# Optimization experiments

Measured on AMD Instinct MI355X. Metric: run time of the kernel, lower is better.

## Reference

```python
import jax, jax.numpy as jnp
import numpy as np
from jax import lax

REL_THR = 0.7
REP_THR = 0.7
EPS = 1e-12


def setup_inputs() -> dict:
    key = jax.random.key(0)
    k1, k2, k3 = jax.random.split(key, 3)
    C, H, W = 128, 768, 1024
    return {
        "features": jax.random.normal(k1, (1, C, H, W), dtype=jnp.float32),
        "clf_w": jax.random.normal(k2, (C, 2), dtype=jnp.float32) * 0.1,
        "clf_b": jnp.zeros((2,), dtype=jnp.float32),
        "sal_w": jax.random.normal(k3, (C, 2), dtype=jnp.float32) * 0.1,
        "sal_b": jnp.zeros((2,), dtype=jnp.float32),
        "max_keypoints": 5000,
    }


def _maxpool3(x):
    # 3x3 stride-1 same-padded max pool on [B, 1, H, W]
    return lax.reduce_window(
        x, -jnp.inf, lax.max,
        window_dimensions=(1, 1, 3, 3),
        window_strides=(1, 1, 1, 1),
        padding=((0, 0), (0, 0), (1, 1), (1, 1)),
    )


def reference(features, clf_w, clf_b, sal_w, sal_b, max_keypoints):
    B, C, H, W = features.shape  # B == 1
    f2 = features ** 2
    # 1x1-conv heads (clf -> reliability logits, sal -> repeatability logits)
    urel = jnp.einsum('bchw,co->bohw', f2, clf_w) + clf_b[None, :, None, None]
    urep = jnp.einsum('bchw,co->bohw', f2, sal_w) + sal_b[None, :, None, None]
    reliability = jax.nn.softmax(urel, axis=1)[:, 1:2]    # [1,1,H,W]
    repeatability = jax.nn.softmax(urep, axis=1)[:, 1:2]  # [1,1,H,W]

    # NonMaxSuppression: local-max + dual threshold
    maxima = (repeatability == _maxpool3(repeatability))
    maxima &= (repeatability >= REP_THR)
    maxima &= (reliability >= REL_THR)

    scores_map = (reliability * repeatability)[0, 0]      # [H, W]
    flat = jnp.where(maxima[0, 0], scores_map, -jnp.inf).reshape(-1)
    scores, idx = lax.top_k(flat, max_keypoints)          # fixed-shape top-K
    y = idx // W
    x = idx % W
    keypoints = jnp.stack([x, y], axis=-1).astype(jnp.float32)  # [K, 2]

    # L2-normalized descriptors gathered at keypoints
    norm = jnp.sqrt(jnp.sum(features * features, axis=1, keepdims=True))
    desc = features / jnp.maximum(norm, EPS)              # [1,C,H,W]
    descriptors = desc[0, :, y, x].T                      # [K, C]
    return keypoints, scores, descriptors
```

## Files before the change

kernel.cpp:

```cpp
#include <hip/hip_runtime.h>
#include <math.h>

#define HH   768
#define WW   1024
#define CC   128
#define HWN  (HH*WW)
#define KTOP 5000
#define CAND_CAP 204800
#define SEL_CAP  8192
#define NBINS    4096
#define BIN_BASE 0x3E800u

#define OFF_REP    0ull
#define OFF_SMAP   3145728ull
#define OFF_CAND   6291456ull
#define OFF_HIST   (OFF_CAND + (unsigned long long)CAND_CAP*8ull)
#define OFF_CTR    (OFF_HIST + (unsigned long long)NBINS*4ull)
#define OFF_SEL    (OFF_CTR + 64ull)
#define OFF_SORTED (OFF_SEL + (unsigned long long)SEL_CAP*8ull)

__device__ __forceinline__ float exp_cr(float x) {
    return (float)::exp((double)x);
}

__global__ void k_zero(unsigned* hist, unsigned* ctr, unsigned* sorted32) {
    int t = blockIdx.x * blockDim.x + threadIdx.x;
    if (t < NBINS) hist[t] = 0u;
    if (t < 16) ctr[t] = 0u;
    if (t < KTOP * 2) sorted32[t] = 0u;
}

__global__ __launch_bounds__(256, 4) void k_maps(const float* __restrict__ f,
                       const float* __restrict__ cw, const float* __restrict__ cb,
                       const float* __restrict__ sw, const float* __restrict__ sb,
                       float* __restrict__ rep, float* __restrict__ smap) {
    __shared__ float w0[CC], w1[CC], w2[CC], w3[CC];
    int t = threadIdx.x;
    if (t < CC) {
        w0[t] = cw[2*t];  w1[t] = cw[2*t+1];
        w2[t] = sw[2*t];  w3[t] = sw[2*t+1];
    }
    __syncthreads();
    int p0 = (blockIdx.x * blockDim.x + t) * 4;
    if (p0 >= HWN) return;
    const float4* fp = (const float4*)(f + p0);
    const long step = HWN / 4;

    float a0[4] = {0,0,0,0}, a1[4] = {0,0,0,0}, a2[4] = {0,0,0,0}, a3[4] = {0,0,0,0};
    float4 A[4], B[4];
    #pragma unroll
    for (int k = 0; k < 4; ++k) A[k] = fp[(long)k * step];

    #define FMA4(REG, CBASE)                                             \
        _Pragma("unroll")                                                \
        for (int k = 0; k < 4; ++k) {                                    \
            int c = (CBASE) + k;                                         \
            float W0 = w0[c], W1 = w1[c], W2 = w2[c], W3 = w3[c];        \
            float vv[4] = {REG[k].x, REG[k].y, REG[k].z, REG[k].w};      \
            _Pragma("unroll")                                            \
            for (int j = 0; j < 4; ++j) {                                \
                float f2 = vv[j] * vv[j];                                \
                a0[j] = fmaf(f2, W0, a0[j]);                             \
                a1[j] = fmaf(f2, W1, a1[j]);                             \
                a2[j] = fmaf(f2, W2, a2[j]);                             \
                a3[j] = fmaf(f2, W3, a3[j]);                             \
            }                                                            \
        }

    for (int c0 = 0; c0 < CC; c0 += 8) {
        #pragma unroll
        for (int k = 0; k < 4; ++k) B[k] = fp[(long)(c0 + 4 + k) * step];
        FMA4(A, c0)
        if (c0 + 8 < CC) {
            #pragma unroll
            for (int k = 0; k < 4; ++k) A[k] = fp[(long)(c0 + 8 + k) * step];
        }
        FMA4(B, c0 + 4)
    }
    #undef FMA4

    float cb0 = cb[0], cb1 = cb[1], sb0 = sb[0], sb1 = sb[1];
    float rp4[4], sm4[4];
    #pragma unroll
    for (int j = 0; j < 4; ++j) {
        float u0 = a0[j] + cb0, u1 = a1[j] + cb1;
        float v0 = a2[j] + sb0, v1 = a3[j] + sb1;
        float mr  = fmaxf(u0, u1);
        float er0 = exp_cr(u0 - mr);
        float er1 = exp_cr(u1 - mr);
        float rel = er1 / (er0 + er1);
        float mp  = fmaxf(v0, v1);
        float ep0 = exp_cr(v0 - mp);
        float ep1 = exp_cr(v1 - mp);
        float rp  = ep1 / (ep0 + ep1);
        rp4[j] = rp;
        sm4[j] = (rel >= 0.7f) ? rel * rp : -1.0f;
    }
    *(float4*)(rep + p0)  = make_float4(rp4[0], rp4[1], rp4[2], rp4[3]);
    *(float4*)(smap + p0) = make_float4(sm4[0], sm4[1], sm4[2], sm4[3]);
}

__global__ void k_nms(const float* __restrict__ rep, const float* __restrict__ smap,
                      unsigned long long* __restrict__ cand, unsigned* __restrict__ ctr,
                      unsigned* __restrict__ hist) {
    int p = blockIdx.x * blockDim.x + threadIdx.x;
    if (p >= HWN) return;
    float r = rep[p];
    if (!(r >= 0.7f)) return;
    float s = smap[p];
    if (!(s >= 0.f)) return;
    int x = p & (WW - 1), y = p >> 10;
    float m = -INFINITY;
    if (y > 0) {
        const float* rr = rep + p - WW;
        if (x > 0)      m = fmaxf(m, rr[-1]);
        m = fmaxf(m, rr[0]);
        if (x < WW - 1) m = fmaxf(m, rr[1]);
    }
    if (x > 0)      m = fmaxf(m, rep[p - 1]);
    if (x < WW - 1) m = fmaxf(m, rep[p + 1]);
    if (y < HH - 1) {
        const float* rr = rep + p + WW;
        if (x > 0)      m = fmaxf(m, rr[-1]);
        m = fmaxf(m, rr[0]);
        if (x < WW - 1) m = fmaxf(m, rr[1]);
    }
    if (r < m) return;
    unsigned pos = atomicAdd(&ctr[0], 1u);
    if (pos < CAND_CAP) {
        unsigned sb = __float_as_uint(s);
        cand[pos] = ((unsigned long long)sb << 32) |
                    (unsigned long long)(0xFFFFFFFFu - (unsigned)p);
        int bin = (int)(sb >> 12) - (int)BIN_BASE;
        bin = bin < 0 ? 0 : (bin > NBINS - 1 ? NBINS - 1 : bin);
        atomicAdd(&hist[bin], 1u);
    }
}

__global__ __launch_bounds__(1024) void k_thr(const unsigned* __restrict__ hist,
                                              unsigned* __restrict__ ctr) {
    __shared__ unsigned ps[1024];
    __shared__ int best;
    int t = threadIdx.x;
    if (t == 0) best = -1;
    unsigned h[4];
    unsigned s = 0;
    #pragma unroll
    for (int k = 0; k < 4; ++k) { h[k] = hist[t*4 + k]; s += h[k]; }
    ps[t] = s;
    __syncthreads();
    for (int off = 1; off < 1024; off <<= 1) {
        unsigned v = (t + off < 1024) ? ps[t + off] : 0u;
        __syncthreads();
        ps[t] += v;
        __syncthreads();
    }
    unsigned above4 = (t < 1023) ? ps[t + 1] : 0u;
    int local = -1;
    unsigned cum = above4;
    #pragma unroll
    for (int k = 3; k >= 0; --k) {
        cum += h[k];
        if (local < 0 && cum >= KTOP) local = t*4 + k;
    }
    if (local >= 0) atomicMax(&best, local);
    __syncthreads();
    if (t == 0) {
        int b = best;
        ctr[2] = (b <= 0) ? 0u : ((unsigned)(b + (int)BIN_BASE) << 12);
    }
}

__global__ void k_select(const unsigned long long* __restrict__ cand,
                         unsigned* __restrict__ ctr, unsigned long long* __restrict__ sel) {
    unsigned n = ctr[0]; if (n > CAND_CAP) n = CAND_CAP;
    unsigned thr = ctr[2];
    int stride = gridDim.x * blockDim.x;
    for (unsigned i = blockIdx.x * blockDim.x + threadIdx.x; i < n; i += stride) {
        unsigned long long k = cand[i];
        if ((unsigned)(k >> 32) >= thr) {
            unsigned pos = atomicAdd(&ctr[1], 1u);
            if (pos < SEL_CAP) sel[pos] = k;
        }
    }
}

__global__ __launch_bounds__(256) void k_rank(const unsigned long long* __restrict__ sel,
                                              const unsigned* __restrict__ ctr,
                                              unsigned long long* __restrict__ sorted) {
    unsigned n = ctr[1]; if (n > SEL_CAP) n = SEL_CAP;
    int wave = (blockIdx.x * 256 + threadIdx.x) >> 6;
    int lane = threadIdx.x & 63;
    int base = wave * 8;
    if (base >= (int)n) return;
    unsigned long long my[8];
    unsigned cnt[8] = {0,0,0,0,0,0,0,0};
    #pragma unroll
    for (int e = 0; e < 8; ++e)
        my[e] = (base + e < (int)n) ? sel[base + e] : ~0ull;
    for (int j = lane; j < (int)n; j += 64) {
        unsigned long long k = sel[j];
        #pragma unroll
        for (int e = 0; e < 8; ++e) cnt[e] += (k > my[e]) ? 1u : 0u;
    }
    #pragma unroll
    for (int e = 0; e < 8; ++e) {
        unsigned c = cnt[e];
        for (int o = 32; o > 0; o >>= 1) c += __shfl_xor(c, o);
        if (lane == 0 && base + e < (int)n && c < KTOP) sorted[c] = my[e];
    }
}

__global__ __launch_bounds__(256) void k_desc(const float* __restrict__ f,
                       const unsigned long long* __restrict__ sorted, float* __restrict__ out) {
    __shared__ float partial[4];
    int half = threadIdx.x >> 7;
    int r = blockIdx.x * 2 + half;
    int c = threadIdx.x & 127;
    if (r >= KTOP) return;
    unsigned long long key = sorted[r];
    unsigned sbits = (unsigned)(key >> 32);
    unsigned p = 0xFFFFFFFFu - (unsigned)(key & 0xFFFFFFFFull);
    if (p >= HWN) p = 0;
    if (c == 0) {
        int x = p & (WW - 1), y = p >> 10;
        out[2*r]        = (float)x;
        out[2*r + 1]    = (float)y;
        out[2*KTOP + r] = __uint_as_float(sbits);
    }
    float v = f[(long)c * HWN + p];
    float ss = v * v;
    for (int o = 32; o > 0; o >>= 1) ss += __shfl_down(ss, o);
    int w = threadIdx.x >> 6;
    if ((threadIdx.x & 63) == 0) partial[w] = ss;
    __syncthreads();
    float tot = partial[half*2] + partial[half*2 + 1];
    float nm = fmaxf(sqrtf(tot), 1e-12f);
    out[3*KTOP + (long)r*CC + c] = v / nm;
}

extern "C" void kernel_launch(void* const* d_in, const int* in_sizes, int n_in,
                              void* d_out, int out_size, void* d_ws, size_t ws_size,
                              hipStream_t stream) {
    const float* feat = (const float*)d_in[0];
    const float* cw   = (const float*)d_in[1];
    const float* cb   = (const float*)d_in[2];
    const float* sw   = (const float*)d_in[3];
    const float* sb   = (const float*)d_in[4];
    float* out = (float*)d_out;

    char* ws = (char*)d_ws;
    float* rep  = (float*)(ws + OFF_REP);
    float* smap = (float*)(ws + OFF_SMAP);
    unsigned long long* cand   = (unsigned long long*)(ws + OFF_CAND);
    unsigned* hist             = (unsigned*)(ws + OFF_HIST);
    unsigned* ctr              = (unsigned*)(ws + OFF_CTR);
    unsigned long long* sel    = (unsigned long long*)(ws + OFF_SEL);
    unsigned long long* sorted = (unsigned long long*)(ws + OFF_SORTED);

    k_zero<<<dim3(64), dim3(256), 0, stream>>>(hist, ctr, (unsigned*)sorted);
    k_maps<<<dim3(HWN / 1024), dim3(256), 0, stream>>>(feat, cw, cb, sw, sb, rep, smap);
    k_nms<<<dim3(HWN / 256), dim3(256), 0, stream>>>(rep, smap, cand, ctr, hist);
    k_thr<<<dim3(1), dim3(1024), 0, stream>>>(hist, ctr);
    k_select<<<dim3(512), dim3(256), 0, stream>>>(cand, ctr, sel);
    k_rank<<<dim3(256), dim3(256), 0, stream>>>(sel, ctr, sorted);
    k_desc<<<dim3((KTOP + 1) / 2), dim3(256), 0, stream>>>(feat, sorted, out);
}
```

Measured before the change: 287.9 us.

## Split channel reduction into four phase kernels with partial-sum planes

Result: slower. 315.6 us (+9.6%).

```diff
diff --git a/kernel.cpp b/kernel.cpp
--- a/kernel.cpp
+++ b/kernel.cpp
@@ -18,6 +18,8 @@
 #define OFF_CTR    (OFF_HIST + (unsigned long long)NBINS*4ull)
 #define OFF_SEL    (OFF_CTR + 64ull)
 #define OFF_SORTED (OFF_SEL + (unsigned long long)SEL_CAP*8ull)
+#define OFF_PART   (16ull*1024*1024)
+#define PART_PLANE 3145728ull
 
 __device__ __forceinline__ float exp_cr(float x) {
     return (float)::exp((double)x);
@@ -30,23 +32,38 @@
     if (t < KTOP * 2) sorted32[t] = 0u;
 }
 
-__global__ __launch_bounds__(256, 4) void k_maps(const float* __restrict__ f,
-                       const float* __restrict__ cw, const float* __restrict__ cb,
-                       const float* __restrict__ sw, const float* __restrict__ sb,
-                       float* __restrict__ rep, float* __restrict__ smap) {
-    __shared__ float w0[CC], w1[CC], w2[CC], w3[CC];
+__global__ __launch_bounds__(256) void k_phase(const float* __restrict__ f,
+                       const float* __restrict__ cw, const float* __restrict__ sw,
+                       float* __restrict__ pa0, float* __restrict__ pa1,
+                       float* __restrict__ pa2, float* __restrict__ pa3,
+                       int c0, int first) {
+    __shared__ float w0[32], w1[32], w2[32], w3[32];
     int t = threadIdx.x;
-    if (t < CC) {
-        w0[t] = cw[2*t];  w1[t] = cw[2*t+1];
-        w2[t] = sw[2*t];  w3[t] = sw[2*t+1];
+    if (t < 32) {
+        w0[t] = cw[2*(c0+t)];  w1[t] = cw[2*(c0+t)+1];
+        w2[t] = sw[2*(c0+t)];  w3[t] = sw[2*(c0+t)+1];
     }
     __syncthreads();
-    int p0 = (blockIdx.x * blockDim.x + t) * 4;
+    int p0 = (blockIdx.x * 256 + t) * 4;
     if (p0 >= HWN) return;
-    const float4* fp = (const float4*)(f + p0);
     const long step = HWN / 4;
-
-    float a0[4] = {0,0,0,0}, a1[4] = {0,0,0,0}, a2[4] = {0,0,0,0}, a3[4] = {0,0,0,0};
+    const float4* fp = (const float4*)(f + p0) + (long)c0 * step;
+
+    float a0[4], a1[4], a2[4], a3[4];
+    if (first) {
+        #pragma unroll
+        for (int j = 0; j < 4; ++j) { a0[j]=0.f; a1[j]=0.f; a2[j]=0.f; a3[j]=0.f; }
+    } else {
+        float4 t0 = *(const float4*)(pa0 + p0);
+        float4 t1 = *(const float4*)(pa1 + p0);
+        float4 t2 = *(const float4*)(pa2 + p0);
+        float4 t3 = *(const float4*)(pa3 + p0);
+        a0[0]=t0.x; a0[1]=t0.y; a0[2]=t0.z; a0[3]=t0.w;
+        a1[0]=t1.x; a1[1]=t1.y; a1[2]=t1.z; a1[3]=t1.w;
+        a2[0]=t2.x; a2[1]=t2.y; a2[2]=t2.z; a2[3]=t2.w;
+        a3[0]=t3.x; a3[1]=t3.y; a3[2]=t3.z; a3[3]=t3.w;
+    }
+
     float4 A[4], B[4];
     #pragma unroll
     for (int k = 0; k < 4; ++k) A[k] = fp[(long)k * step];
@@ -67,18 +84,37 @@
             }                                                            \
         }
 
-    for (int c0 = 0; c0 < CC; c0 += 8) {
+    for (int cc = 0; cc < 32; cc += 8) {
         #pragma unroll
-        for (int k = 0; k < 4; ++k) B[k] = fp[(long)(c0 + 4 + k) * step];
-        FMA4(A, c0)
-        if (c0 + 8 < CC) {
+        for (int k = 0; k < 4; ++k) B[k] = fp[(long)(cc + 4 + k) * step];
+        FMA4(A, cc)
+        if (cc + 8 < 32) {
             #pragma unroll
-            for (int k = 0; k < 4; ++k) A[k] = fp[(long)(c0 + 8 + k) * step];
+            for (int k = 0; k < 4; ++k) A[k] = fp[(long)(cc + 8 + k) * step];
         }
-        FMA4(B, c0 + 4)
+        FMA4(B, cc + 4)
     }
     #undef FMA4
 
+    *(float4*)(pa0 + p0) = make_float4(a0[0], a0[1], a0[2], a0[3]);
+    *(float4*)(pa1 + p0) = make_float4(a1[0], a1[1], a1[2], a1[3]);
+    *(float4*)(pa2 + p0) = make_float4(a2[0], a2[1], a2[2], a2[3]);
+    *(float4*)(pa3 + p0) = make_float4(a3[0], a3[1], a3[2], a3[3]);
+}
+
+__global__ __launch_bounds__(256) void k_soft(const float* __restrict__ pa0,
+                       const float* __restrict__ pa1, const float* __restrict__ pa2,
+                       const float* __restrict__ pa3,
+                       const float* __restrict__ cb, const float* __restrict__ sb,
+                       float* __restrict__ rep, float* __restrict__ smap) {
+    int p0 = (blockIdx.x * 256 + threadIdx.x) * 4;
+    if (p0 >= HWN) return;
+    float4 t0 = *(const float4*)(pa0 + p0);
+    float4 t1 = *(const float4*)(pa1 + p0);
+    float4 t2 = *(const float4*)(pa2 + p0);
+    float4 t3 = *(const float4*)(pa3 + p0);
+    float a0[4] = {t0.x,t0.y,t0.z,t0.w}, a1[4] = {t1.x,t1.y,t1.z,t1.w};
+    float a2[4] = {t2.x,t2.y,t2.z,t2.w}, a3[4] = {t3.x,t3.y,t3.z,t3.w};
     float cb0 = cb[0], cb1 = cb[1], sb0 = sb[0], sb1 = sb[1];
     float rp4[4], sm4[4];
     #pragma unroll
@@ -257,9 +293,17 @@
     unsigned* ctr              = (unsigned*)(ws + OFF_CTR);
     unsigned long long* sel    = (unsigned long long*)(ws + OFF_SEL);
     unsigned long long* sorted = (unsigned long long*)(ws + OFF_SORTED);
+    float* pa0 = (float*)(ws + OFF_PART);
+    float* pa1 = (float*)(ws + OFF_PART + 1*PART_PLANE);
+    float* pa2 = (float*)(ws + OFF_PART + 2*PART_PLANE);
+    float* pa3 = (float*)(ws + OFF_PART + 3*PART_PLANE);
 
     k_zero<<<dim3(64), dim3(256), 0, stream>>>(hist, ctr, (unsigned*)sorted);
-    k_maps<<<dim3(HWN / 1024), dim3(256), 0, stream>>>(feat, cw, cb, sw, sb, rep, smap);
+    for (int ph = 0; ph < 4; ++ph) {
+        k_phase<<<dim3(HWN / 1024), dim3(256), 0, stream>>>(
+            feat, cw, sw, pa0, pa1, pa2, pa3, ph * 32, ph == 0 ? 1 : 0);
+    }
+    k_soft<<<dim3(HWN / 1024), dim3(256), 0, stream>>>(pa0, pa1, pa2, pa3, cb, sb, rep, smap);
     k_nms<<<dim3(HWN / 256), dim3(256), 0, stream>>>(rep, smap, cand, ctr, hist);
     k_thr<<<dim3(1), dim3(1024), 0, stream>>>(hist, ctr);
     k_select<<<dim3(512), dim3(256), 0, stream>>>(cand, ctr, sel);
```

## Fold zeroing into k_maps and batch descriptor gathers per block

Applied to the files above, without the earlier changes.

Result: no change. 289.2 us (+0.5%).

```diff
diff --git a/kernel.cpp b/kernel.cpp
--- a/kernel.cpp
+++ b/kernel.cpp
@@ -10,6 +10,7 @@
 #define SEL_CAP  8192
 #define NBINS    4096
 #define BIN_BASE 0x3E800u
+#define DESC_KP  64
 
 #define OFF_REP    0ull
 #define OFF_SMAP   3145728ull
@@ -23,25 +24,25 @@
     return (float)::exp((double)x);
 }
 
-__global__ void k_zero(unsigned* hist, unsigned* ctr, unsigned* sorted32) {
-    int t = blockIdx.x * blockDim.x + threadIdx.x;
-    if (t < NBINS) hist[t] = 0u;
-    if (t < 16) ctr[t] = 0u;
-    if (t < KTOP * 2) sorted32[t] = 0u;
-}
-
 __global__ __launch_bounds__(256, 4) void k_maps(const float* __restrict__ f,
                        const float* __restrict__ cw, const float* __restrict__ cb,
                        const float* __restrict__ sw, const float* __restrict__ sb,
-                       float* __restrict__ rep, float* __restrict__ smap) {
+                       float* __restrict__ rep, float* __restrict__ smap,
+                       unsigned* __restrict__ hist, unsigned* __restrict__ ctr,
+                       unsigned* __restrict__ sorted32) {
     __shared__ float w0[CC], w1[CC], w2[CC], w3[CC];
     int t = threadIdx.x;
+    if (blockIdx.x == 0) {
+        for (int i = t; i < NBINS; i += 256) hist[i] = 0u;
+        if (t < 16) ctr[t] = 0u;
+        for (int i = t; i < KTOP * 2; i += 256) sorted32[i] = 0u;
+    }
     if (t < CC) {
         w0[t] = cw[2*t];  w1[t] = cw[2*t+1];
         w2[t] = sw[2*t];  w3[t] = sw[2*t+1];
     }
     __syncthreads();
-    int p0 = (blockIdx.x * blockDim.x + t) * 4;
+    int p0 = (blockIdx.x * 256 + t) * 4;
     if (p0 >= HWN) return;
     const float4* fp = (const float4*)(f + p0);
     const long step = HWN / 4;
@@ -212,31 +213,53 @@
 }
 
 __global__ __launch_bounds__(256) void k_desc(const float* __restrict__ f,
-                       const unsigned long long* __restrict__ sorted, float* __restrict__ out) {
-    __shared__ float partial[4];
-    int half = threadIdx.x >> 7;
-    int r = blockIdx.x * 2 + half;
-    int c = threadIdx.x & 127;
-    if (r >= KTOP) return;
-    unsigned long long key = sorted[r];
-    unsigned sbits = (unsigned)(key >> 32);
-    unsigned p = 0xFFFFFFFFu - (unsigned)(key & 0xFFFFFFFFull);
-    if (p >= HWN) p = 0;
-    if (c == 0) {
-        int x = p & (WW - 1), y = p >> 10;
-        out[2*r]        = (float)x;
-        out[2*r + 1]    = (float)y;
-        out[2*KTOP + r] = __uint_as_float(sbits);
-    }
-    float v = f[(long)c * HWN + p];
-    float ss = v * v;
-    for (int o = 32; o > 0; o >>= 1) ss += __shfl_down(ss, o);
-    int w = threadIdx.x >> 6;
-    if ((threadIdx.x & 63) == 0) partial[w] = ss;
-    __syncthreads();
-    float tot = partial[half*2] + partial[half*2 + 1];
-    float nm = fmaxf(sqrtf(tot), 1e-12f);
-    out[3*KTOP + (long)r*CC + c] = v / nm;
+                       const unsigned long long* __restrict__ sorted,
+                       float* __restrict__ out) {
+    __shared__ float vbuf[DESC_KP][CC + 1];
+    __shared__ float psum[4][DESC_KP];
+    __shared__ float nrm[DESC_KP];
+    __shared__ unsigned pix[DESC_KP];
+    int t = threadIdx.x, w = t >> 6, lane = t & 63;
+    int rbase = blockIdx.x * DESC_KP;
+
+    if (t < DESC_KP) {
+        int r = rbase + t;
+        unsigned long long key = (r < KTOP) ? sorted[r] : 0ull;
+        unsigned sbits = (unsigned)(key >> 32);
+        unsigned p = 0xFFFFFFFFu - (unsigned)(key & 0xFFFFFFFFull);
+        if (p >= HWN) p = 0;
+        pix[t] = p;
+        if (r < KTOP) {
+            out[2*r]        = (float)(p & (WW - 1));
+            out[2*r + 1]    = (float)(p >> 10);
+            out[2*KTOP + r] = __uint_as_float(sbits);
+        }
+    }
+    __syncthreads();
+    unsigned p = pix[lane];
+    float ss = 0.f;
+    #pragma unroll 8
+    for (int cc = 0; cc < 32; ++cc) {
+        int c = w * 32 + cc;
+        float v = f[(long)c * HWN + p];
+        vbuf[lane][c] = v;
+        ss = fmaf(v, v, ss);
+    }
+    psum[w][lane] = ss;
+    __syncthreads();
+    if (t < DESC_KP) {
+        float tot = psum[0][t] + psum[1][t] + psum[2][t] + psum[3][t];
+        nrm[t] = fmaxf(sqrtf(tot), 1e-12f);
+    }
+    __syncthreads();
+    int kp2 = t >> 7;
+    int c   = t & 127;
+    for (int it = 0; it < DESC_KP / 2; ++it) {
+        int kp = it * 2 + kp2;
+        int r  = rbase + kp;
+        if (r < KTOP)
+            out[3*KTOP + (long)r*CC + c] = vbuf[kp][c] / nrm[kp];
+    }
 }
 
 extern "C" void kernel_launch(void* const* d_in, const int* in_sizes, int n_in,
@@ -258,11 +281,11 @@
     unsigned long long* sel    = (unsigned long long*)(ws + OFF_SEL);
     unsigned long long* sorted = (unsigned long long*)(ws + OFF_SORTED);
 
-    k_zero<<<dim3(64), dim3(256), 0, stream>>>(hist, ctr, (unsigned*)sorted);
-    k_maps<<<dim3(HWN / 1024), dim3(256), 0, stream>>>(feat, cw, cb, sw, sb, rep, smap);
+    k_maps<<<dim3(HWN / 1024), dim3(256), 0, stream>>>(feat, cw, cb, sw, sb, rep, smap,
+                                                       hist, ctr, (unsigned*)sorted);
     k_nms<<<dim3(HWN / 256), dim3(256), 0, stream>>>(rep, smap, cand, ctr, hist);
     k_thr<<<dim3(1), dim3(1024), 0, stream>>>(hist, ctr);
     k_select<<<dim3(512), dim3(256), 0, stream>>>(cand, ctr, sel);
     k_rank<<<dim3(256), dim3(256), 0, stream>>>(sel, ctr, sorted);
-    k_desc<<<dim3((KTOP + 1) / 2), dim3(256), 0, stream>>>(feat, sorted, out);
-}
+    k_desc<<<dim3((KTOP + DESC_KP - 1) / DESC_KP), dim3(256), 0, stream>>>(feat, sorted, out);
+}
```
